# Performance work log

Measured on AMD Instinct MI355X. Metric: run time of the kernel, lower is better.

The kernel has to match this reference:

```python
import jax, jax.numpy as jnp
import numpy as np
import math

B = 512
EMB = 512
CLASSNUM = 70722
M = 0.4
H = 0.333
S = 64.0
EPS = 1e-3


def setup_inputs() -> dict:
    key = jax.random.key(0)
    k1, k2, k3, k4, k5 = jax.random.split(key, 5)
    embbedings = jax.random.normal(k1, (B, EMB), dtype=jnp.float32)
    # feature norms: positive, realistic range ~[1, 30)
    norms = jax.random.uniform(k2, (B, 1), dtype=jnp.float32) * 29.0 + 1.0
    label = jax.random.randint(k3, (B,), 0, CLASSNUM, dtype=jnp.int64)
    class_sample_num_ = jax.random.uniform(k4, (B,), dtype=jnp.float32) * 9.0 + 1.0
    kernel = jax.random.normal(k5, (EMB, CLASSNUM), dtype=jnp.float32)
    return {
        "embbedings": embbedings,
        "norms": norms,
        "label": label,
        "class_sample_num_": class_sample_num_,
        "kernel": kernel,
    }


def reference(embbedings, norms, label, class_sample_num_, kernel):
    # l2-normalize kernel columns (axis=0)
    kernel_norm = kernel / jnp.linalg.norm(kernel, axis=0, keepdims=True)
    cosine = jnp.matmul(embbedings, kernel_norm)  # [B, C]
    cosine = jnp.clip(cosine, -1.0 + EPS, 1.0 - EPS)

    # detached margin scaler path (torch uses .detach / no_grad)
    safe_norms = jnp.clip(norms, 0.001, 100.0)
    safe_norms = safe_norms / (class_sample_num_[:, None] + 0.001)
    safe_norms = jnp.clip(safe_norms, 0.001, 100.0)
    safe_norms = jax.lax.stop_gradient(safe_norms)

    mean = jnp.mean(safe_norms)
    std = jnp.std(safe_norms, ddof=1)  # torch.std is unbiased
    # t_alpha = 1.0 => batch stats are exactly this batch's mean/std
    batch_mean, batch_std = mean, std

    margin_scaler = (safe_norms - batch_mean) / (batch_std + EPS)
    margin_scaler = jnp.clip(margin_scaler * H, -1.0, 1.0)  # [B, 1]
    ms = margin_scaler[:, 0]  # [B]

    rows = jnp.arange(B)
    lab = label.astype(jnp.int32)

    # angular margin: theta_m = clip(theta + onehot * (-m*ms))
    theta = jnp.arccos(cosine)
    theta = theta.at[rows, lab].add(-M * ms)
    theta_m = jnp.clip(theta, EPS, math.pi - EPS)
    cosine2 = jnp.cos(theta_m)

    # additive margin at the label column: g_add = m + m*ms
    cosine2 = cosine2.at[rows, lab].add(-(M + M * ms))

    return cosine2 * S
```

## Files before the change

kernel.cpp:

```cpp
#include <hip/hip_runtime.h>
#include <hip/hip_bf16.h>
#include <math.h>

#define CLASSNUM 70722
#define BATCH 512
#define EMBD 512
#define M_C 0.4f
#define H_C 0.333f
#define S_C 64.0f
#define EPS_C 0.001f
#define PI_F 3.14159265358979f

typedef __bf16 bf16_t;
typedef __bf16 bf16x8 __attribute__((ext_vector_type(8)));
typedef float f32x4 __attribute__((ext_vector_type(4)));

__device__ __forceinline__ float clampf(float x, float lo, float hi) {
    return fminf(fmaxf(x, lo), hi);
}

__device__ __forceinline__ void async_copy16(const bf16_t* g, bf16_t* l) {
    __builtin_amdgcn_global_load_lds(
        (const __attribute__((address_space(1))) unsigned int*)g,
        (__attribute__((address_space(3))) unsigned int*)l, 16, 0, 0);
}


__global__ __launch_bounds__(256) void prep_kernel(
    const float* __restrict__ emb, const float* __restrict__ norms,
    const float* __restrict__ csn, bf16_t* __restrict__ Aws,
    float* __restrict__ msw)
{
    __shared__ float sred[256];
    const int tid = threadIdx.x;
    if (blockIdx.x == 0) {
        float s0, s1;
        {
            float sn = clampf(norms[tid], 0.001f, 100.0f);
            sn = sn / (csn[tid] + 0.001f);
            s0 = clampf(sn, 0.001f, 100.0f);
        }
        {
            float sn = clampf(norms[tid + 256], 0.001f, 100.0f);
            sn = sn / (csn[tid + 256] + 0.001f);
            s1 = clampf(sn, 0.001f, 100.0f);
        }
        sred[tid] = s0 + s1;
        __syncthreads();
        for (int off = 128; off > 0; off >>= 1) {
            if (tid < off) sred[tid] += sred[tid + off];
            __syncthreads();
        }
        const float mean = sred[0] * (1.0f / 512.0f);
        __syncthreads();
        const float d0 = s0 - mean, d1 = s1 - mean;
        sred[tid] = d0 * d0 + d1 * d1;
        __syncthreads();
        for (int off = 128; off > 0; off >>= 1) {
            if (tid < off) sred[tid] += sred[tid + off];
            __syncthreads();
        }
        const float stdv = sqrtf(sred[0] * (1.0f / 511.0f));
        const float inv = 1.0f / (stdv + EPS_C);
        msw[tid]       = clampf(d0 * inv * H_C, -1.0f, 1.0f);
        msw[tid + 256] = clampf(d1 * inv * H_C, -1.0f, 1.0f);
    } else {
        const int G = (blockIdx.x - 1) * 256 + tid;
        const int kt = G >> 11;
        const int rem = G & 2047;
        const int m = rem >> 2;
        const int q = rem & 3;
        const int qs = q ^ ((m >> 1) & 3);
        const float* src = emb + m * EMBD + kt * 32 + qs * 8;
        const float4 v0 = *(const float4*)src;
        const float4 v1 = *(const float4*)(src + 4);
        bf16x8 bw;
        bw[0] = (bf16_t)v0.x; bw[1] = (bf16_t)v0.y;
        bw[2] = (bf16_t)v0.z; bw[3] = (bf16_t)v0.w;
        bw[4] = (bf16_t)v1.x; bw[5] = (bf16_t)v1.y;
        bw[6] = (bf16_t)v1.z; bw[7] = (bf16_t)v1.w;
        *(bf16x8*)(Aws + (size_t)G * 8) = bw;
    }
}

__global__ __launch_bounds__(64) void lab_kernel(
    const float* __restrict__ emb, const int* __restrict__ label,
    const float* __restrict__ kmat, const float* __restrict__ msw,
    float* __restrict__ labout)
{
    const int b = blockIdx.x;
    const int l = threadIdx.x;
    const int lab = label[b];
    const float* col = kmat + lab;
    const float* e = emb + b * EMBD;
    float dot = 0.0f, ss = 0.0f;
    for (int k = l; k < EMBD; k += 64) {
        const float kv = col[(size_t)k * CLASSNUM];
        const float ev = e[k];
        dot = fmaf(ev, kv, dot);
        ss  = fmaf(kv, kv, ss);
    }
    for (int off = 32; off > 0; off >>= 1) {
        dot += __shfl_down(dot, off);
        ss  += __shfl_down(ss, off);
    }
    if (l == 0) {
        float c = dot / sqrtf(ss);
        c = clampf(c, -1.0f + EPS_C, 1.0f - EPS_C);
        const float msv = msw[b];
        float th = acosf(c) - M_C * msv;
        th = clampf(th, EPS_C, PI_F - EPS_C);
        labout[b] = (cosf(th) - (M_C + M_C * msv)) * S_C;
    }
}

__global__ __launch_bounds__(256, 2) void gemm_kernel(
    const bf16_t* __restrict__ Aws, const float* __restrict__ Kmat,
    float* __restrict__ out)
{
    __shared__ bf16_t Alds[2][512 * 32];
    __shared__ bf16_t Blds[2][64 * 40];
    __shared__ float red[256];
    __shared__ float invn[64];

    const int tid  = threadIdx.x;
    const int lane = tid & 63;
    const int wave = tid >> 6;
    const int quad = lane >> 4;
    const int r16  = lane & 15;
    const int n0   = blockIdx.x * 64;

    const int bc = tid & 63;
    const int bh = tid >> 6;
    const bool nv = (n0 + bc) < CLASSNUM;
    const float* bp = Kmat + (size_t)(n0 + bc);

    f32x4 acc[8][4];
    const f32x4 zero = {0.0f, 0.0f, 0.0f, 0.0f};
#pragma unroll
    for (int i = 0; i < 8; ++i)
#pragma unroll
        for (int j = 0; j < 4; ++j) acc[i][j] = zero;

    float ssq = 0.0f;
    float bv[8];

#pragma unroll
    for (int j = 0; j < 8; ++j)
        bv[j] = nv ? bp[(size_t)(bh * 8 + j) * CLASSNUM] : 0.0f;
#pragma unroll
    for (int i = 0; i < 8; ++i)
        async_copy16(Aws + i * 2048 + wave * 512 + lane * 8,
                     &Alds[0][i * 2048 + wave * 512]);
    {
        bf16x8 bw;
#pragma unroll
        for (int j = 0; j < 8; ++j) {
            const float v = bv[j];
            ssq = fmaf(v, v, ssq);
            bw[j] = (bf16_t)v;
        }
        *(bf16x8*)&Blds[0][bc * 40 + bh * 8] = bw;
    }

    for (int it = 0; it < 16; ++it) {
        const int buf = it & 1;
        __syncthreads();

        if (it < 15) {
            const size_t kb = (size_t)((it + 1) * 32 + bh * 8) * CLASSNUM;
#pragma unroll
            for (int j = 0; j < 8; ++j)
                bv[j] = nv ? bp[kb + (size_t)j * CLASSNUM] : 0.0f;
            const bf16_t* gs = Aws + (size_t)(it + 1) * 16384;
#pragma unroll
            for (int i = 0; i < 8; ++i)
                async_copy16(gs + i * 2048 + wave * 512 + lane * 8,
                             &Alds[buf ^ 1][i * 2048 + wave * 512]);
        }

        bf16x8 bfr[4];
#pragma unroll
        for (int ni = 0; ni < 4; ++ni)
            bfr[ni] = *(const bf16x8*)&Blds[buf][(ni * 16 + r16) * 40 + quad * 8];
#pragma unroll
        for (int mi = 0; mi < 8; ++mi) {
            const int row = wave * 128 + mi * 16 + r16;
            const int swz = (row >> 1) & 3;
            const bf16x8 af = *(const bf16x8*)
                &Alds[buf][row * 32 + ((quad ^ swz) << 3)];
#pragma unroll
            for (int ni = 0; ni < 4; ++ni)
                acc[mi][ni] = __builtin_amdgcn_mfma_f32_16x16x32_bf16(
                    af, bfr[ni], acc[mi][ni], 0, 0, 0);
        }

        if (it < 15) {
            bf16x8 bw;
#pragma unroll
            for (int j = 0; j < 8; ++j) {
                const float v = bv[j];
                ssq = fmaf(v, v, ssq);
                bw[j] = (bf16_t)v;
            }
            *(bf16x8*)&Blds[buf ^ 1][bc * 40 + bh * 8] = bw;
        }
    }

    red[tid] = ssq;
    __syncthreads();
    if (tid < 64) {
        const float s = red[tid] + red[tid + 64] + red[tid + 128] + red[tid + 192];
        invn[tid] = (s > 0.0f) ? (1.0f / sqrtf(s)) : 0.0f;
    }
    __syncthreads();

#pragma unroll
    for (int mi = 0; mi < 8; ++mi) {
        const int row = wave * 128 + mi * 16 + quad * 4;
#pragma unroll
        for (int rr = 0; rr < 4; ++rr) {
            float* orow = out + (size_t)(row + rr) * CLASSNUM;
#pragma unroll
            for (int ni = 0; ni < 4; ++ni) {
                const int col_loc = ni * 16 + r16;
                const int col = n0 + col_loc;
                if (col < CLASSNUM) {
                    const float c = clampf(acc[mi][ni][rr] * invn[col_loc],
                                           -1.0f + EPS_C, 1.0f - EPS_C);
                    orow[col] = c * S_C;
                }
            }
        }
    }
}

__global__ __launch_bounds__(512) void scatter_kernel(
    const int* __restrict__ label, const float* __restrict__ labout,
    float* __restrict__ out)
{
    const int t = threadIdx.x;
    out[(size_t)t * CLASSNUM + label[t]] = labout[t];
}

extern "C" void kernel_launch(void* const* d_in, const int* in_sizes, int n_in,
                              void* d_out, int out_size, void* d_ws, size_t ws_size,
                              hipStream_t stream)
{
    const float* emb   = (const float*)d_in[0];
    const float* norms = (const float*)d_in[1];
    const int*   label = (const int*)d_in[2];
    const float* csn   = (const float*)d_in[3];
    const float* kmat  = (const float*)d_in[4];
    float* out = (float*)d_out;

    const size_t A_BYTES = (size_t)BATCH * EMBD * sizeof(bf16_t);
    if (ws_size < A_BYTES + 4096) return;
    bf16_t* Aws   = (bf16_t*)d_ws;
    float* msw    = (float*)((char*)d_ws + A_BYTES);
    float* labout = (float*)((char*)d_ws + A_BYTES + 2048);

    prep_kernel<<<129, 256, 0, stream>>>(emb, norms, csn, Aws, msw);
    lab_kernel<<<BATCH, 64, 0, stream>>>(emb, label, kmat, msw, labout);
    const int nblk = (CLASSNUM + 63) / 64;
    gemm_kernel<<<nblk, 256, 0, stream>>>(Aws, kmat, out);
    scatter_kernel<<<1, 512, 0, stream>>>(label, labout, out);
}
```

Before: 365.2 us.

## Fuse prep and label kernels, register-pipeline GEMM without LDS, fuse scatter

Merges the margin-statistics, bf16 conversion and label-column computations into one launch, with each label block recomputing batch mean and std itself. The GEMM drops LDS staging. Each of 8 waves loads its A fragments, pre-laid out in MFMA order, and its B kernel columns straight from global memory into registers, double-buffered across K steps. The label-column fix-up moves into the GEMM epilogue, which removes the separate scatter launch. The aim is to cut launch count, barriers and LDS traffic, at the cost of more per-thread global loads, higher register pressure and redundant statistics work in 512 blocks.

```diff
diff --git a/kernel.cpp b/kernel.cpp
--- a/kernel.cpp
+++ b/kernel.cpp
@@ -1,5 +1,4 @@
 #include <hip/hip_runtime.h>
-#include <hip/hip_bf16.h>
 #include <math.h>
 
 #define CLASSNUM 70722
@@ -19,59 +18,25 @@
     return fminf(fmaxf(x, lo), hi);
 }
 
-__device__ __forceinline__ void async_copy16(const bf16_t* g, bf16_t* l) {
-    __builtin_amdgcn_global_load_lds(
-        (const __attribute__((address_space(1))) unsigned int*)g,
-        (__attribute__((address_space(3))) unsigned int*)l, 16, 0, 0);
-}
-
-
-__global__ __launch_bounds__(256) void prep_kernel(
+__global__ __launch_bounds__(256) void prep_lab_kernel(
     const float* __restrict__ emb, const float* __restrict__ norms,
-    const float* __restrict__ csn, bf16_t* __restrict__ Aws,
-    float* __restrict__ msw)
+    const float* __restrict__ csn, const int* __restrict__ label,
+    const float* __restrict__ kmat, bf16_t* __restrict__ Aws,
+    float* __restrict__ labout)
 {
-    __shared__ float sred[256];
+    __shared__ float red[256];
     const int tid = threadIdx.x;
-    if (blockIdx.x == 0) {
-        float s0, s1;
-        {
-            float sn = clampf(norms[tid], 0.001f, 100.0f);
-            sn = sn / (csn[tid] + 0.001f);
-            s0 = clampf(sn, 0.001f, 100.0f);
-        }
-        {
-            float sn = clampf(norms[tid + 256], 0.001f, 100.0f);
-            sn = sn / (csn[tid + 256] + 0.001f);
-            s1 = clampf(sn, 0.001f, 100.0f);
-        }
-        sred[tid] = s0 + s1;
-        __syncthreads();
-        for (int off = 128; off > 0; off >>= 1) {
-            if (tid < off) sred[tid] += sred[tid + off];
-            __syncthreads();
-        }
-        const float mean = sred[0] * (1.0f / 512.0f);
-        __syncthreads();
-        const float d0 = s0 - mean, d1 = s1 - mean;
-        sred[tid] = d0 * d0 + d1 * d1;
-        __syncthreads();
-        for (int off = 128; off > 0; off >>= 1) {
-            if (tid < off) sred[tid] += sred[tid + off];
-            __syncthreads();
-        }
-        const float stdv = sqrtf(sred[0] * (1.0f / 511.0f));
-        const float inv = 1.0f / (stdv + EPS_C);
-        msw[tid]       = clampf(d0 * inv * H_C, -1.0f, 1.0f);
-        msw[tid + 256] = clampf(d1 * inv * H_C, -1.0f, 1.0f);
-    } else {
-        const int G = (blockIdx.x - 1) * 256 + tid;
+    const int bi = blockIdx.x;
+
+    if (bi < 128) {
+        const int G = bi * 256 + tid;
         const int kt = G >> 11;
         const int rem = G & 2047;
-        const int m = rem >> 2;
-        const int q = rem & 3;
-        const int qs = q ^ ((m >> 1) & 3);
-        const float* src = emb + m * EMBD + kt * 32 + qs * 8;
+        const int rg = rem >> 6;
+        const int lane = rem & 63;
+        const int row = rg * 16 + (lane & 15);
+        const int k0 = kt * 32 + (lane >> 4) * 8;
+        const float* src = emb + row * EMBD + k0;
         const float4 v0 = *(const float4*)src;
         const float4 v1 = *(const float4*)(src + 4);
         bf16x8 bw;
@@ -80,167 +45,221 @@
         bw[4] = (bf16_t)v1.x; bw[5] = (bf16_t)v1.y;
         bw[6] = (bf16_t)v1.z; bw[7] = (bf16_t)v1.w;
         *(bf16x8*)(Aws + (size_t)G * 8) = bw;
-    }
-}
-
-__global__ __launch_bounds__(64) void lab_kernel(
-    const float* __restrict__ emb, const int* __restrict__ label,
-    const float* __restrict__ kmat, const float* __restrict__ msw,
-    float* __restrict__ labout)
-{
-    const int b = blockIdx.x;
-    const int l = threadIdx.x;
+        return;
+    }
+
+    const int b = bi - 128;
+
+    float s0, s1;
+    {
+        float sn = clampf(norms[tid], 0.001f, 100.0f);
+        sn = sn / (csn[tid] + 0.001f);
+        s0 = clampf(sn, 0.001f, 100.0f);
+    }
+    {
+        float sn = clampf(norms[tid + 256], 0.001f, 100.0f);
+        sn = sn / (csn[tid + 256] + 0.001f);
+        s1 = clampf(sn, 0.001f, 100.0f);
+    }
+    red[tid] = s0 + s1;
+    __syncthreads();
+    for (int off = 128; off > 0; off >>= 1) {
+        if (tid < off) red[tid] += red[tid + off];
+        __syncthreads();
+    }
+    const float mean = red[0] * (1.0f / 512.0f);
+    __syncthreads();
+    const float d0 = s0 - mean, d1 = s1 - mean;
+    red[tid] = d0 * d0 + d1 * d1;
+    __syncthreads();
+    for (int off = 128; off > 0; off >>= 1) {
+        if (tid < off) red[tid] += red[tid + off];
+        __syncthreads();
+    }
+    const float stdv = sqrtf(red[0] * (1.0f / 511.0f));
+    __syncthreads();
+
     const int lab = label[b];
     const float* col = kmat + lab;
     const float* e = emb + b * EMBD;
     float dot = 0.0f, ss = 0.0f;
-    for (int k = l; k < EMBD; k += 64) {
+#pragma unroll
+    for (int k = tid; k < EMBD; k += 256) {
         const float kv = col[(size_t)k * CLASSNUM];
         const float ev = e[k];
         dot = fmaf(ev, kv, dot);
         ss  = fmaf(kv, kv, ss);
     }
-    for (int off = 32; off > 0; off >>= 1) {
-        dot += __shfl_down(dot, off);
-        ss  += __shfl_down(ss, off);
-    }
-    if (l == 0) {
-        float c = dot / sqrtf(ss);
+    red[tid] = dot;
+    __syncthreads();
+    for (int off = 128; off > 0; off >>= 1) {
+        if (tid < off) red[tid] += red[tid + off];
+        __syncthreads();
+    }
+    const float dotT = red[0];
+    __syncthreads();
+    red[tid] = ss;
+    __syncthreads();
+    for (int off = 128; off > 0; off >>= 1) {
+        if (tid < off) red[tid] += red[tid + off];
+        __syncthreads();
+    }
+    if (tid == 0) {
+        const float ssT = red[0];
+        float c = dotT / sqrtf(ssT);
         c = clampf(c, -1.0f + EPS_C, 1.0f - EPS_C);
-        const float msv = msw[b];
+        float snb = clampf(norms[b], 0.001f, 100.0f);
+        snb = snb / (csn[b] + 0.001f);
+        snb = clampf(snb, 0.001f, 100.0f);
+        const float msv = clampf((snb - mean) / (stdv + EPS_C) * H_C, -1.0f, 1.0f);
         float th = acosf(c) - M_C * msv;
         th = clampf(th, EPS_C, PI_F - EPS_C);
         labout[b] = (cosf(th) - (M_C + M_C * msv)) * S_C;
     }
 }
 
-__global__ __launch_bounds__(256, 2) void gemm_kernel(
+
+#define LOADB(kt, bv) do {                                              \
+    const size_t kb_ = (size_t)((kt) * 32) * CLASSNUM;                  \
+    _Pragma("unroll")                                                   \
+    for (int ni_ = 0; ni_ < 4; ++ni_) {                                 \
+        _Pragma("unroll")                                               \
+        for (int j_ = 0; j_ < 8; ++j_)                                  \
+            bv[ni_][j_] = bq[ni_][kb_ + (size_t)j_ * CLASSNUM];         \
+    }                                                                   \
+} while (0)
+
+#define LOADA(kt, af) do {                                              \
+    const bf16x8* ap_ = (const bf16x8*)Aws                              \
+        + (((kt) * 32 + wave * 4) * 64 + lane);                         \
+    _Pragma("unroll")                                                   \
+    for (int mi_ = 0; mi_ < 4; ++mi_) af[mi_] = ap_[mi_ * 64];          \
+} while (0)
+
+#define CVTB(bv, bfr) do {                                              \
+    _Pragma("unroll")                                                   \
+    for (int ni_ = 0; ni_ < 4; ++ni_) {                                 \
+        _Pragma("unroll")                                               \
+        for (int j_ = 0; j_ < 8; ++j_) {                                \
+            const float v_ = bv[ni_][j_];                               \
+            ssq[ni_] = fmaf(v_, v_, ssq[ni_]);                          \
+            bfr[ni_][j_] = (bf16_t)v_;                                  \
+        }                                                               \
+    }                                                                   \
+} while (0)
+
+#define DOMFMA(af, bfr) do {                                            \
+    _Pragma("unroll")                                                   \
+    for (int mi_ = 0; mi_ < 4; ++mi_) {                                 \
+        _Pragma("unroll")                                               \
+        for (int ni_ = 0; ni_ < 4; ++ni_)                               \
+            acc[mi_][ni_] = __builtin_amdgcn_mfma_f32_16x16x32_bf16(    \
+                af[mi_], bfr[ni_], acc[mi_][ni_], 0, 0, 0);             \
+    }                                                                   \
+} while (0)
+
+__global__ __launch_bounds__(512, 2) void gemm_kernel(
     const bf16_t* __restrict__ Aws, const float* __restrict__ Kmat,
+    const int* __restrict__ label, const float* __restrict__ labout,
     float* __restrict__ out)
 {
-    __shared__ bf16_t Alds[2][512 * 32];
-    __shared__ bf16_t Blds[2][64 * 40];
-    __shared__ float red[256];
-    __shared__ float invn[64];
-
-    const int tid  = threadIdx.x;
+    __shared__ int   lab_s[BATCH];
+    __shared__ float lo_s[BATCH];
+    const int tid = threadIdx.x;
+    lab_s[tid] = label[tid];
+    lo_s[tid]  = labout[tid];
+    __syncthreads();
+
     const int lane = tid & 63;
     const int wave = tid >> 6;
+    const int r16  = lane & 15;
     const int quad = lane >> 4;
-    const int r16  = lane & 15;
     const int n0   = blockIdx.x * 64;
 
-    const int bc = tid & 63;
-    const int bh = tid >> 6;
-    const bool nv = (n0 + bc) < CLASSNUM;
-    const float* bp = Kmat + (size_t)(n0 + bc);
-
-    f32x4 acc[8][4];
+    const float* bq[4];
+    bool cok[4];
+#pragma unroll
+    for (int ni = 0; ni < 4; ++ni) {
+        int c = n0 + ni * 16 + r16;
+        cok[ni] = (c < CLASSNUM);
+        c = cok[ni] ? c : (CLASSNUM - 1);
+        bq[ni] = Kmat + (size_t)(quad * 8) * CLASSNUM + c;
+    }
+
+    f32x4 acc[4][4];
     const f32x4 zero = {0.0f, 0.0f, 0.0f, 0.0f};
 #pragma unroll
-    for (int i = 0; i < 8; ++i)
+    for (int i = 0; i < 4; ++i)
 #pragma unroll
         for (int j = 0; j < 4; ++j) acc[i][j] = zero;
-
-    float ssq = 0.0f;
-    float bv[8];
-
-#pragma unroll
-    for (int j = 0; j < 8; ++j)
-        bv[j] = nv ? bp[(size_t)(bh * 8 + j) * CLASSNUM] : 0.0f;
-#pragma unroll
-    for (int i = 0; i < 8; ++i)
-        async_copy16(Aws + i * 2048 + wave * 512 + lane * 8,
-                     &Alds[0][i * 2048 + wave * 512]);
-    {
-        bf16x8 bw;
-#pragma unroll
-        for (int j = 0; j < 8; ++j) {
-            const float v = bv[j];
-            ssq = fmaf(v, v, ssq);
-            bw[j] = (bf16_t)v;
+    float ssq[4] = {0.0f, 0.0f, 0.0f, 0.0f};
+
+    float bvA[4][8], bvB[4][8];
+    bf16x8 afC[4], afN[4];
+
+    LOADB(0, bvA);
+    LOADB(1, bvB);
+    LOADA(0, afC);
+
+#pragma unroll 1
+    for (int p = 0; p < 7; ++p) {
+        {
+            bf16x8 bfr[4];
+            CVTB(bvA, bfr);
+            LOADB(2 * p + 2, bvA);
+            LOADA(2 * p + 1, afN);
+            DOMFMA(afC, bfr);
         }
-        *(bf16x8*)&Blds[0][bc * 40 + bh * 8] = bw;
-    }
-
-    for (int it = 0; it < 16; ++it) {
-        const int buf = it & 1;
-        __syncthreads();
-
-        if (it < 15) {
-            const size_t kb = (size_t)((it + 1) * 32 + bh * 8) * CLASSNUM;
-#pragma unroll
-            for (int j = 0; j < 8; ++j)
-                bv[j] = nv ? bp[kb + (size_t)j * CLASSNUM] : 0.0f;
-            const bf16_t* gs = Aws + (size_t)(it + 1) * 16384;
-#pragma unroll
-            for (int i = 0; i < 8; ++i)
-                async_copy16(gs + i * 2048 + wave * 512 + lane * 8,
-                             &Alds[buf ^ 1][i * 2048 + wave * 512]);
+        {
+            bf16x8 bfr[4];
+            CVTB(bvB, bfr);
+            LOADB(2 * p + 3, bvB);
+            LOADA(2 * p + 2, afC);
+            DOMFMA(afN, bfr);
         }
-
+    }
+    {
         bf16x8 bfr[4];
-#pragma unroll
-        for (int ni = 0; ni < 4; ++ni)
-            bfr[ni] = *(const bf16x8*)&Blds[buf][(ni * 16 + r16) * 40 + quad * 8];
-#pragma unroll
-        for (int mi = 0; mi < 8; ++mi) {
-            const int row = wave * 128 + mi * 16 + r16;
-            const int swz = (row >> 1) & 3;
-            const bf16x8 af = *(const bf16x8*)
-                &Alds[buf][row * 32 + ((quad ^ swz) << 3)];
-#pragma unroll
-            for (int ni = 0; ni < 4; ++ni)
-                acc[mi][ni] = __builtin_amdgcn_mfma_f32_16x16x32_bf16(
-                    af, bfr[ni], acc[mi][ni], 0, 0, 0);
-        }
-
-        if (it < 15) {
-            bf16x8 bw;
-#pragma unroll
-            for (int j = 0; j < 8; ++j) {
-                const float v = bv[j];
-                ssq = fmaf(v, v, ssq);
-                bw[j] = (bf16_t)v;
-            }
-            *(bf16x8*)&Blds[buf ^ 1][bc * 40 + bh * 8] = bw;
-        }
-    }
-
-    red[tid] = ssq;
-    __syncthreads();
-    if (tid < 64) {
-        const float s = red[tid] + red[tid + 64] + red[tid + 128] + red[tid + 192];
-        invn[tid] = (s > 0.0f) ? (1.0f / sqrtf(s)) : 0.0f;
-    }
-    __syncthreads();
-
-#pragma unroll
-    for (int mi = 0; mi < 8; ++mi) {
-        const int row = wave * 128 + mi * 16 + quad * 4;
+        CVTB(bvA, bfr);
+        LOADA(15, afN);
+        DOMFMA(afC, bfr);
+    }
+    {
+        bf16x8 bfr[4];
+        CVTB(bvB, bfr);
+        DOMFMA(afN, bfr);
+    }
+
+    float invn[4];
+#pragma unroll
+    for (int ni = 0; ni < 4; ++ni) {
+        float s = ssq[ni];
+        s += __shfl_xor(s, 16);
+        s += __shfl_xor(s, 32);
+        invn[ni] = (s > 0.0f) ? (1.0f / sqrtf(s)) : 0.0f;
+    }
+
+#pragma unroll
+    for (int mi = 0; mi < 4; ++mi) {
 #pragma unroll
         for (int rr = 0; rr < 4; ++rr) {
-            float* orow = out + (size_t)(row + rr) * CLASSNUM;
+            const int row = wave * 64 + mi * 16 + quad * 4 + rr;
+            const int labc = lab_s[row];
+            const float lov = lo_s[row];
+            float* orow = out + (size_t)row * CLASSNUM;
 #pragma unroll
             for (int ni = 0; ni < 4; ++ni) {
-                const int col_loc = ni * 16 + r16;
-                const int col = n0 + col_loc;
-                if (col < CLASSNUM) {
-                    const float c = clampf(acc[mi][ni][rr] * invn[col_loc],
+                if (cok[ni]) {
+                    const int col = n0 + ni * 16 + r16;
+                    const float c = clampf(acc[mi][ni][rr] * invn[ni],
                                            -1.0f + EPS_C, 1.0f - EPS_C);
-                    orow[col] = c * S_C;
+                    float v = c * S_C;
+                    if (labc == col) v = lov;
+                    orow[col] = v;
                 }
             }
         }
     }
-}
-
-__global__ __launch_bounds__(512) void scatter_kernel(
-    const int* __restrict__ label, const float* __restrict__ labout,
-    float* __restrict__ out)
-{
-    const int t = threadIdx.x;
-    out[(size_t)t * CLASSNUM + label[t]] = labout[t];
 }
 
 extern "C" void kernel_launch(void* const* d_in, const int* in_sizes, int n_in,
@@ -257,12 +276,10 @@
     const size_t A_BYTES = (size_t)BATCH * EMBD * sizeof(bf16_t);
     if (ws_size < A_BYTES + 4096) return;
     bf16_t* Aws   = (bf16_t*)d_ws;
-    float* msw    = (float*)((char*)d_ws + A_BYTES);
-    float* labout = (float*)((char*)d_ws + A_BYTES + 2048);
-
-    prep_kernel<<<129, 256, 0, stream>>>(emb, norms, csn, Aws, msw);
-    lab_kernel<<<BATCH, 64, 0, stream>>>(emb, label, kmat, msw, labout);
+    float* labout = (float*)((char*)d_ws + A_BYTES);
+
+    prep_lab_kernel<<<128 + BATCH, 256, 0, stream>>>(
+        emb, norms, csn, label, kmat, Aws, labout);
     const int nblk = (CLASSNUM + 63) / 64;
-    gemm_kernel<<<nblk, 256, 0, stream>>>(Aws, kmat, out);
-    scatter_kernel<<<1, 512, 0, stream>>>(label, labout, out);
-}
+    gemm_kernel<<<nblk, 512, 0, stream>>>(Aws, kmat, label, labout, out);
+}
```

New measurement: 382.8 us. 1.05x slower.
